# Optimization experiments

Measured on AMD Instinct MI355X. Metric: run time of the kernel, lower is better.

The kernel has to match this reference:

```python
import jax, jax.numpy as jnp
import numpy as np

B, N, C = 2, 9216, 512
HEAD, SR = 8, 4
R = 32  # lora rank
SCALING = 4.0 / 32.0  # alpha / r


def setup_inputs() -> dict:
    key = jax.random.key(0)
    ks = jax.random.split(key, 16)
    s = 0.02
    inp = {
        "x": jax.random.normal(ks[0], (B, N, C), jnp.float32),
        "w_q": jax.random.normal(ks[1], (C, C), jnp.float32) * s,
        "b_q": jnp.zeros((C,), jnp.float32),
        "w_kv": jax.random.normal(ks[2], (2 * C, C), jnp.float32) * s,
        "b_kv": jnp.zeros((2 * C,), jnp.float32),
        "w_proj": jax.random.normal(ks[3], (C, C), jnp.float32) * s,
        "b_proj": jnp.zeros((C,), jnp.float32),
        "w_sr": jax.random.normal(ks[4], (C, C, SR, SR), jnp.float32) * s,
        "b_sr": jnp.zeros((C,), jnp.float32),
        "ln_g": jnp.ones((C,), jnp.float32),
        "ln_b": jnp.zeros((C,), jnp.float32),
        "lora_A_q": jax.random.normal(ks[5], (R, C), jnp.float32) * s,
        "lora_B_q": jax.random.normal(ks[6], (C, R), jnp.float32) * s,
        "lora_A_v": jax.random.normal(ks[7], (R, C), jnp.float32) * s,
        "lora_B_v": jax.random.normal(ks[8], (C, R), jnp.float32) * s,
        "H": 96,
        "W": 96,
    }
    return inp


def reference(x, w_q, b_q, w_kv, b_kv, w_proj, b_proj, w_sr, b_sr,
              ln_g, ln_b, lora_A_q, lora_B_q, lora_A_v, lora_B_v, H, W):
    b, n, c = x.shape
    d = c // HEAD
    # q = Linear(x) + LoRA(x) * scaling
    q = x @ w_q.T + b_q + ((x @ lora_A_q.T) @ lora_B_q.T) * SCALING
    q = q.reshape(b, n, HEAD, d).transpose(0, 2, 1, 3)  # (B, h, N, d)
    # spatial reduction: Conv2d(dim, dim, sr, sr) then LayerNorm
    xi = x.transpose(0, 2, 1).reshape(b, c, H, W)
    xs = jax.lax.conv_general_dilated(
        xi, w_sr, window_strides=(SR, SR), padding='VALID',
        dimension_numbers=('NCHW', 'OIHW', 'NCHW'))
    xs = xs + b_sr[None, :, None, None]
    xs = xs.reshape(b, c, -1).transpose(0, 2, 1)  # (B, Nkv, C)
    mu = jnp.mean(xs, axis=-1, keepdims=True)
    var = jnp.var(xs, axis=-1, keepdims=True)
    xs = (xs - mu) * jax.lax.rsqrt(var + 1e-5) * ln_g + ln_b
    # k, v
    kv = (xs @ w_kv.T + b_kv).reshape(b, -1, 2, HEAD, d).transpose(2, 0, 3, 1, 4)
    k, v = kv[0], kv[1]  # (B, h, Nkv, d)
    lv = ((xs @ lora_A_v.T) @ lora_B_v.T) * SCALING  # (B, Nkv, C)
    # faithful to torch: raw memory reshape, NOT a head-transpose
    v = v + lv.reshape(b, HEAD, -1, d)
    # attention
    attn = jax.nn.softmax(jnp.einsum('bhnd,bhmd->bhnm', q, k) * (d ** -0.5), axis=-1)
    out = jnp.einsum('bhnm,bhmd->bhnd', attn, v).transpose(0, 2, 1, 3).reshape(b, n, c)
    return out @ w_proj.T + b_proj
```

## Files before the change

kernel.cpp:

```cpp
#include <hip/hip_runtime.h>

typedef __attribute__((ext_vector_type(8))) __bf16 bf16x8;
typedef __attribute__((ext_vector_type(4))) float f32x4;
typedef __attribute__((ext_vector_type(4))) unsigned int u32x4;
typedef __attribute__((ext_vector_type(2))) unsigned int u32x2;

#define MFMA16(a, b, c) __builtin_amdgcn_mfma_f32_16x16x32_bf16((a), (b), (c), 0, 0, 0)
#define QSCALE 0.18033688011112042f

__device__ __forceinline__ bool input_is_f32(const void* ln_g) {
    return ((const unsigned*)ln_g)[0] == 0x3F800000u;
}

__device__ __forceinline__ float rdf(const void* p, long i, bool f32) {
    return f32 ? ((const float*)p)[i] : (float)((const __bf16*)p)[i];
}

__device__ __forceinline__ void conv_big(const void* s, __bf16* d, long base, bool f) {
    long i = base + (long)threadIdx.x * 8;
    if (f) {
        f32x4 a = ((const f32x4*)s)[i / 4];
        f32x4 b = ((const f32x4*)s)[i / 4 + 1];
        bf16x8 o;
        #pragma unroll
        for (int j = 0; j < 4; ++j) { o[j] = (__bf16)a[j]; o[4 + j] = (__bf16)b[j]; }
        *(bf16x8*)(d + i) = o;
    } else {
        *(u32x4*)(d + i) = ((const u32x4*)s)[i / 8];
    }
}

__device__ __forceinline__ void conv_small(const void* s, __bf16* d, int n, bool f) {
    int i = threadIdx.x * 4;
    if (i < n) {
        #pragma unroll
        for (int j = 0; j < 4; ++j)
            d[i + j] = f ? (__bf16)((const float*)s)[i + j] : ((const __bf16*)s)[i + j];
    }
}

__global__ void convert_prep_kernel(const void* x, const void* w_kv, const void* w_proj,
                                    const void* b_q, const void* b_kv, const void* b_proj,
                                    const void* b_sr, const void* ln_g, const void* ln_b,
                                    const void* __restrict__ w_q,
                                    const void* __restrict__ Aq, const void* __restrict__ Bq,
                                    const void* __restrict__ Av, const void* __restrict__ Bv,
                                    const void* __restrict__ w_sr,
                                    __bf16* x_b, __bf16* w_kv_b, __bf16* w_proj_b,
                                    __bf16* b_q_b, __bf16* b_kv_b, __bf16* b_proj_b,
                                    __bf16* b_sr_b, __bf16* ln_g_b, __bf16* ln_b_b,
                                    __bf16* __restrict__ w_q_eff, __bf16* __restrict__ w_lv,
                                    __bf16* __restrict__ w_sr_t) {
    const bool f = input_is_f32(ln_g);
    int blk = blockIdx.x;
    if (blk < 4608)      conv_big(x, x_b, (long)blk * 2048, f);
    else if (blk < 4864) conv_big(w_kv, w_kv_b, (long)(blk - 4608) * 2048, f);
    else if (blk < 4992) conv_big(w_proj, w_proj_b, (long)(blk - 4864) * 2048, f);
    else if (blk == 4992) conv_small(b_q, b_q_b, 512, f);
    else if (blk == 4993) conv_small(b_kv, b_kv_b, 1024, f);
    else if (blk == 4994) conv_small(b_proj, b_proj_b, 512, f);
    else if (blk == 4995) conv_small(b_sr, b_sr_b, 512, f);
    else if (blk == 4996) conv_small(ln_g, ln_g_b, 512, f);
    else if (blk == 4997) conv_small(ln_b, ln_b_b, 512, f);
    else {
        int tid = (blk - 4998) * 256 + threadIdx.x;
        if (tid < 262144) {
            int o = tid >> 9, c = tid & 511;
            float acc = 0.f;
            #pragma unroll 8
            for (int r = 0; r < 32; ++r)
                acc += rdf(Bq, o * 32 + r, f) * rdf(Aq, r * 512 + c, f);
            w_q_eff[tid] = (__bf16)(rdf(w_q, tid, f) + 0.125f * acc);
        } else if (tid < 524288) {
            int t = tid - 262144;
            int o = t >> 9, c = t & 511;
            float acc = 0.f;
            #pragma unroll 8
            for (int r = 0; r < 32; ++r)
                acc += rdf(Bv, o * 32 + r, f) * rdf(Av, r * 512 + c, f);
            w_lv[t] = (__bf16)(0.125f * acc);
        } else if (tid < 786432) {
            int t = tid - 524288;
            int o = t >> 9, i = t & 511;
            #pragma unroll
            for (int p = 0; p < 16; ++p)
                w_sr_t[(size_t)o * 8192 + p * 512 + i] = (__bf16)rdf(w_sr, (long)t * 16 + p, f);
        }
    }
}

__global__ __launch_bounds__(256, 4) void qconv_gemm(const __bf16* __restrict__ x,
                                                     const __bf16* __restrict__ Wt,
                                                     const __bf16* __restrict__ Wq,
                                                     const __bf16* __restrict__ bq,
                                                     float* __restrict__ part,
                                                     __bf16* __restrict__ q_t) {
    __shared__ __attribute__((aligned(16))) char lds[36864];
    char* As = lds;
    char* Bs = lds + 18432;
    const int tid = threadIdx.x;
    const int swz = (blockIdx.x & 7) * 144 + (blockIdx.x >> 3);
    const bool isconv = (swz & 1) == 0;
    const int hid = swz >> 1;
    const int w = tid >> 6, lane = tid & 63;
    const int wm = (w >> 1) << 6, wn = (w & 1) << 6;
    const int lr = lane & 15, lg = lane >> 4;
    const int srow = tid >> 1, half = tid & 1;

    int m0, n0, kzv = 0;
    const __bf16 *Arow, *Brow;
    if (isconv) {
        kzv = hid / 36;
        int r = hid % 36;
        int nb = r / 9, mb = r % 9;
        m0 = mb << 7; n0 = nb << 7;
        int m = m0 + srow;
        int bb = m >= 576 ? 1 : 0;
        int rem = m - bb * 576;
        int oy = rem / 24;
        int ox = rem - oy * 24;
        int ky = kzv >> 2, kx = kzv & 3;
        Arow = x + ((size_t)bb * 9216 + (size_t)(oy * 384 + ky * 96 + ox * 4 + kx)) * 512
               + half * 32;
        Brow = Wt + (size_t)(n0 + srow) * 8192 + kzv * 512 + half * 32;
    } else {
        int mb = hid >> 2, nb = hid & 3;
        m0 = mb << 7; n0 = nb << 7;
        Arow = x + (size_t)(m0 + srow) * 512 + half * 32;
        Brow = Wq + (size_t)(n0 + srow) * 512 + half * 32;
    }
    char* Asw = As + srow * 144 + half * 64;
    char* Bsw = Bs + srow * 144 + half * 64;

    f32x4 acc[4][4] = {};

    u32x4 a0 = *(const u32x4*)(Arow);
    u32x4 a1 = *(const u32x4*)(Arow + 8);
    u32x4 a2 = *(const u32x4*)(Arow + 16);
    u32x4 a3 = *(const u32x4*)(Arow + 24);
    u32x4 b0 = *(const u32x4*)(Brow);
    u32x4 b1 = *(const u32x4*)(Brow + 8);
    u32x4 b2 = *(const u32x4*)(Brow + 16);
    u32x4 b3 = *(const u32x4*)(Brow + 24);

    for (int k0 = 0; k0 < 512; k0 += 64) {
        __syncthreads();
        *(u32x4*)(Asw) = a0;
        *(u32x4*)(Asw + 16) = a1;
        *(u32x4*)(Asw + 32) = a2;
        *(u32x4*)(Asw + 48) = a3;
        *(u32x4*)(Bsw) = b0;
        *(u32x4*)(Bsw + 16) = b1;
        *(u32x4*)(Bsw + 32) = b2;
        *(u32x4*)(Bsw + 48) = b3;
        __syncthreads();
        int kn = k0 + 64;
        if (kn < 512) {
            a0 = *(const u32x4*)(Arow + kn);
            a1 = *(const u32x4*)(Arow + kn + 8);
            a2 = *(const u32x4*)(Arow + kn + 16);
            a3 = *(const u32x4*)(Arow + kn + 24);
            b0 = *(const u32x4*)(Brow + kn);
            b1 = *(const u32x4*)(Brow + kn + 8);
            b2 = *(const u32x4*)(Brow + kn + 16);
            b3 = *(const u32x4*)(Brow + kn + 24);
        }
        bf16x8 a[4][2], b[4][2];
        #pragma unroll
        for (int i = 0; i < 4; ++i)
            #pragma unroll
            for (int ks = 0; ks < 2; ++ks)
                a[i][ks] = *(const bf16x8*)(As + (wm + i * 16 + lr) * 144 + ks * 64 + lg * 16);
        #pragma unroll
        for (int j = 0; j < 4; ++j)
            #pragma unroll
            for (int ks = 0; ks < 2; ++ks)
                b[j][ks] = *(const bf16x8*)(Bs + (wn + j * 16 + lr) * 144 + ks * 64 + lg * 16);
        #pragma unroll
        for (int i = 0; i < 4; ++i)
            #pragma unroll
            for (int j = 0; j < 4; ++j)
                #pragma unroll
                for (int ks = 0; ks < 2; ++ks)
                    acc[i][j] = MFMA16(a[i][ks], b[j][ks], acc[i][j]);
    }

    if (isconv) {
        float* pout = part + (size_t)kzv * 589824;
        #pragma unroll
        for (int j = 0; j < 4; ++j) {
            int col = n0 + wn + j * 16 + lr;
            #pragma unroll
            for (int i = 0; i < 4; ++i) {
                int rb = m0 + wm + i * 16 + lg * 4;
                #pragma unroll
                for (int r = 0; r < 4; ++r)
                    pout[(size_t)(rb + r) * 512 + col] = acc[i][j][r];
            }
        }
    } else {
        #pragma unroll
        for (int j = 0; j < 4; ++j) {
            int col = n0 + wn + j * 16 + lr;
            float bv = (float)bq[col];
            #pragma unroll
            for (int i = 0; i < 4; ++i) {
                int rb = m0 + wm + i * 16 + lg * 4;
                #pragma unroll
                for (int r = 0; r < 4; ++r) {
                    int grow = rb + r;
                    int b_ = grow >= 9216 ? 1 : 0;
                    int nn = grow - b_ * 9216;
                    q_t[(((size_t)(b_ * 8 + (col >> 6))) * 9216 + nn) * 64 + (col & 63)] =
                        (__bf16)((acc[i][j][r] + bv) * QSCALE);
                }
            }
        }
    }
}

__global__ __launch_bounds__(256, 4) void proj_gemm(const __bf16* __restrict__ A,
                                                    const __bf16* __restrict__ Bt,
                                                    const __bf16* __restrict__ bias,
                                                    float* __restrict__ out) {
    __shared__ __attribute__((aligned(16))) char lds[27648];
    char* As = lds;
    char* Bs = lds + 9216;
    const int tid = threadIdx.x;
    const int swz = (blockIdx.x & 7) * 144 + (blockIdx.x >> 3);
    const int m0 = (swz >> 2) << 6, n0 = (swz & 3) << 7;
    const int w = tid >> 6, lane = tid & 63;
    const int wm = (w >> 1) << 5, wn = (w & 1) << 6;
    const int lr = lane & 15, lg = lane >> 4;

    f32x4 acc[2][4] = {};

    const int srow = tid >> 1, half = tid & 1;
    const bool doA = tid < 128;
    const __bf16* Arow = A + (size_t)(m0 + (srow & 63)) * 512 + half * 32;
    const __bf16* Brow = Bt + (size_t)(n0 + srow) * 512 + half * 32;
    char* Asw = As + (srow & 63) * 144 + half * 64;
    char* Bsw = Bs + srow * 144 + half * 64;

    u32x4 a0{}, a1{}, a2{}, a3{};
    if (doA) {
        a0 = *(const u32x4*)(Arow);
        a1 = *(const u32x4*)(Arow + 8);
        a2 = *(const u32x4*)(Arow + 16);
        a3 = *(const u32x4*)(Arow + 24);
    }
    u32x4 b0 = *(const u32x4*)(Brow);
    u32x4 b1 = *(const u32x4*)(Brow + 8);
    u32x4 b2 = *(const u32x4*)(Brow + 16);
    u32x4 b3 = *(const u32x4*)(Brow + 24);

    for (int k0 = 0; k0 < 512; k0 += 64) {
        __syncthreads();
        if (doA) {
            *(u32x4*)(Asw) = a0;
            *(u32x4*)(Asw + 16) = a1;
            *(u32x4*)(Asw + 32) = a2;
            *(u32x4*)(Asw + 48) = a3;
        }
        *(u32x4*)(Bsw) = b0;
        *(u32x4*)(Bsw + 16) = b1;
        *(u32x4*)(Bsw + 32) = b2;
        *(u32x4*)(Bsw + 48) = b3;
        __syncthreads();
        int kn = k0 + 64;
        if (kn < 512) {
            if (doA) {
                a0 = *(const u32x4*)(Arow + kn);
                a1 = *(const u32x4*)(Arow + kn + 8);
                a2 = *(const u32x4*)(Arow + kn + 16);
                a3 = *(const u32x4*)(Arow + kn + 24);
            }
            b0 = *(const u32x4*)(Brow + kn);
            b1 = *(const u32x4*)(Brow + kn + 8);
            b2 = *(const u32x4*)(Brow + kn + 16);
            b3 = *(const u32x4*)(Brow + kn + 24);
        }
        bf16x8 a[2][2], b[4][2];
        #pragma unroll
        for (int i = 0; i < 2; ++i)
            #pragma unroll
            for (int ks = 0; ks < 2; ++ks)
                a[i][ks] = *(const bf16x8*)(As + (wm + i * 16 + lr) * 144 + ks * 64 + lg * 16);
        #pragma unroll
        for (int j = 0; j < 4; ++j)
            #pragma unroll
            for (int ks = 0; ks < 2; ++ks)
                b[j][ks] = *(const bf16x8*)(Bs + (wn + j * 16 + lr) * 144 + ks * 64 + lg * 16);
        #pragma unroll
        for (int i = 0; i < 2; ++i)
            #pragma unroll
            for (int j = 0; j < 4; ++j)
                #pragma unroll
                for (int ks = 0; ks < 2; ++ks)
                    acc[i][j] = MFMA16(a[i][ks], b[j][ks], acc[i][j]);
    }

    #pragma unroll
    for (int j = 0; j < 4; ++j) {
        int col = n0 + wn + j * 16 + lr;
        float bv = (float)bias[col];
        #pragma unroll
        for (int i = 0; i < 2; ++i) {
            int rb = m0 + wm + i * 16 + lg * 4;
            #pragma unroll
            for (int r = 0; r < 4; ++r)
                out[(size_t)(rb + r) * 512 + col] = acc[i][j][r] + bv;
        }
    }
}

__global__ __launch_bounds__(64) void lnorm(const float* __restrict__ parts,
                                            const __bf16* __restrict__ b_sr,
                                            const __bf16* __restrict__ g,
                                            const __bf16* __restrict__ be,
                                            __bf16* __restrict__ out) {
    int row = blockIdx.x;
    int lane = threadIdx.x;
    const float* xr = parts + (size_t)row * 512;
    float v[8], s = 0.f, sq = 0.f;
    #pragma unroll
    for (int i = 0; i < 8; ++i) {
        int c = lane + i * 64;
        float t = (float)b_sr[c];
        #pragma unroll
        for (int sp = 0; sp < 16; ++sp)
            t += xr[(size_t)sp * 589824 + c];
        v[i] = t;
        s += t;
        sq += t * t;
    }
    #pragma unroll
    for (int d = 1; d < 64; d <<= 1) {
        s += __shfl_xor(s, d);
        sq += __shfl_xor(sq, d);
    }
    float mean = s * (1.0f / 512.0f);
    float var = sq * (1.0f / 512.0f) - mean * mean;
    float rstd = rsqrtf(var + 1e-5f);
    __bf16* orow = out + (size_t)row * 512;
    #pragma unroll
    for (int i = 0; i < 8; ++i) {
        int c = lane + i * 64;
        orow[c] = (__bf16)((v[i] - mean) * rstd * (float)g[c] + (float)be[c]);
    }
}

__global__ __launch_bounds__(256) void kv_gemm(const __bf16* __restrict__ xs,
                                               const __bf16* __restrict__ w_kv,
                                               const __bf16* __restrict__ w_lv,
                                               const __bf16* __restrict__ b_kv,
                                               __bf16* __restrict__ k_t,
                                               float* __restrict__ v_raw,
                                               __bf16* __restrict__ lv) {
    __shared__ __attribute__((aligned(16))) char lds[18432];
    char* As = lds;
    char* Bs = lds + 9216;
    const int tid = threadIdx.x;
    const int m0 = blockIdx.x << 6, n0 = blockIdx.y << 6;
    const int w = tid >> 6, lane = tid & 63;
    const int wm = (w >> 1) << 5, wn = (w & 1) << 5;
    const int lr = lane & 15, lg = lane >> 4;

    const int srow = tid >> 2, sc = tid & 3;
    const __bf16* arow = xs + (size_t)(m0 + srow) * 512;
    const __bf16* brow = (n0 < 1024) ? (w_kv + (size_t)(n0 + srow) * 512)
                                     : (w_lv + (size_t)(n0 - 1024 + srow) * 512);

    u32x4 pav[2], pbv[2];
    #pragma unroll
    for (int j = 0; j < 2; ++j) {
        int c = sc + j * 4;
        pav[j] = *(const u32x4*)(arow + c * 8);
        pbv[j] = *(const u32x4*)(brow + c * 8);
    }

    f32x4 acc[2][2] = {};
    for (int k0 = 0; k0 < 512; k0 += 64) {
        __syncthreads();
        #pragma unroll
        for (int j = 0; j < 2; ++j) {
            int c = sc + j * 4;
            *(u32x4*)(As + srow * 144 + c * 16) = pav[j];
            *(u32x4*)(Bs + srow * 144 + c * 16) = pbv[j];
        }
        __syncthreads();
        int kn = k0 + 64;
        if (kn < 512) {
            #pragma unroll
            for (int j = 0; j < 2; ++j) {
                int c = sc + j * 4;
                pav[j] = *(const u32x4*)(arow + kn + c * 8);
                pbv[j] = *(const u32x4*)(brow + kn + c * 8);
            }
        }
        bf16x8 a[2][2], b[2][2];
        #pragma unroll
        for (int i = 0; i < 2; ++i)
            #pragma unroll
            for (int ks = 0; ks < 2; ++ks) {
                a[i][ks] = *(const bf16x8*)(As + (wm + i * 16 + lr) * 144 + ks * 64 + lg * 16);
                b[i][ks] = *(const bf16x8*)(Bs + (wn + i * 16 + lr) * 144 + ks * 64 + lg * 16);
            }
        #pragma unroll
        for (int i = 0; i < 2; ++i)
            #pragma unroll
            for (int j = 0; j < 2; ++j)
                #pragma unroll
                for (int ks = 0; ks < 2; ++ks)
                    acc[i][j] = MFMA16(a[i][ks], b[j][ks], acc[i][j]);
    }
    #pragma unroll
    for (int j = 0; j < 2; ++j) {
        int col = n0 + wn + j * 16 + lr;
        float bv = (col < 1024) ? (float)b_kv[col] : 0.0f;
        #pragma unroll
        for (int i = 0; i < 2; ++i) {
            int rb = m0 + wm + i * 16 + lg * 4;
            #pragma unroll
            for (int r = 0; r < 4; ++r) {
                int grow = rb + r;
                float val = acc[i][j][r] + bv;
                int b_ = grow >= 576 ? 1 : 0;
                int mm = grow - b_ * 576;
                if (col < 512) {
                    int h = col >> 6, dd = col & 63;
                    k_t[(((size_t)(b_ * 8 + h)) * 576 + mm) * 64 + dd] = (__bf16)val;
                } else if (col < 1024) {
                    v_raw[((size_t)b_ * 576 + mm) * 512 + (col - 512)] = val;
                } else {
                    lv[((size_t)b_ * 576 + mm) * 512 + (col - 1024)] = (__bf16)val;
                }
            }
        }
    }
}

__global__ void v_fixup(const float* __restrict__ v_raw, const __bf16* __restrict__ lv,
                        __bf16* __restrict__ vT) {
    int tid = blockIdx.x * 256 + threadIdx.x;
    if (tid >= 589824) return;
    int mm = tid % 576;
    int rest = tid / 576;
    int dd = rest & 63;
    int bh = rest >> 6;
    int b_ = bh >> 3, h = bh & 7;
    int flat = h * 36864 + mm * 64 + dd;
    int n2 = flat >> 9, c2 = flat & 511;
    float val = v_raw[((size_t)b_ * 576 + mm) * 512 + h * 64 + dd] +
                (float)lv[((size_t)b_ * 576 + n2) * 512 + c2];
    vT[tid] = (__bf16)val;
}

__global__ __launch_bounds__(256, 4) void attn_kernel(const __bf16* __restrict__ q_t,
                                                      const __bf16* __restrict__ k_t,
                                                      const __bf16* __restrict__ vT,
                                                      __bf16* __restrict__ attnv) {
    __shared__ __attribute__((aligned(16))) char lds[18432];
    char* Ks = lds;
    char* Vs = lds + 9216;
    const int tid = threadIdx.x;
    const int w = tid >> 6, lane = tid & 63;
    const int lr = lane & 15, lg = lane >> 4;
    const int bh = blockIdx.y;
    const int qrow0 = (blockIdx.x << 7) + (w << 5);

    bf16x8 qf[2][2];
    #pragma unroll
    for (int qb = 0; qb < 2; ++qb)
        #pragma unroll
        for (int ks = 0; ks < 2; ++ks)
            qf[qb][ks] = *(const bf16x8*)(q_t + ((size_t)bh * 9216 + qrow0 + qb * 16 + lr) * 64 +
                                          ks * 32 + lg * 8);

    bf16x8 ones;
    #pragma unroll
    for (int j = 0; j < 8; ++j) ones[j] = (__bf16)1.0f;

    f32x4 oacc[2][4] = {};
    f32x4 lacc[2] = {};

    const int rr = tid >> 2, q4 = tid & 3;
    const __bf16* kg = k_t + ((size_t)bh * 576 + rr) * 64 + q4 * 16;
    char* ksw = Ks + rr * 144 + q4 * 32;
    const __bf16* vg = vT + ((size_t)bh * 64 + rr) * 576 + q4 * 16;
    char* vsw = Vs + rr * 144;
    const int offA = ((q4 & 1) << 3) | ((q4 >> 1) << 6);

    u32x4 k0v = *(const u32x4*)(kg);
    u32x4 k1v = *(const u32x4*)(kg + 8);
    u32x4 v0v = *(const u32x4*)(vg);
    u32x4 v1v = *(const u32x4*)(vg + 8);

    for (int kv0 = 0; kv0 < 576; kv0 += 64) {
        __syncthreads();
        *(u32x4*)(ksw) = k0v;
        *(u32x4*)(ksw + 16) = k1v;
        {
            u32x2 t0, t1, t2, t3;
            t0[0] = v0v[0]; t0[1] = v0v[1];
            t1[0] = v0v[2]; t1[1] = v0v[3];
            t2[0] = v1v[0]; t2[1] = v1v[1];
            t3[0] = v1v[2]; t3[1] = v1v[3];
            *(u32x2*)(vsw + offA) = t0;
            *(u32x2*)(vsw + offA + 16) = t1;
            *(u32x2*)(vsw + offA + 32) = t2;
            *(u32x2*)(vsw + offA + 48) = t3;
        }
        __syncthreads();
        int kvn = kv0 + 64;
        if (kvn < 576) {
            k0v = *(const u32x4*)(kg + (size_t)kvn * 64);
            k1v = *(const u32x4*)(kg + (size_t)kvn * 64 + 8);
            v0v = *(const u32x4*)(vg + kvn);
            v1v = *(const u32x4*)(vg + kvn + 8);
        }

        #pragma unroll
        for (int ch = 0; ch < 2; ++ch) {
            bf16x8 kf[2][2];
            #pragma unroll
            for (int kb = 0; kb < 2; ++kb)
                #pragma unroll
                for (int ks = 0; ks < 2; ++ks)
                    kf[kb][ks] = *(const bf16x8*)(Ks + ((ch * 2 + kb) * 16 + lr) * 144 +
                                                  ks * 64 + lg * 16);
            f32x4 st[2][2] = {};
            #pragma unroll
            for (int kb = 0; kb < 2; ++kb)
                #pragma unroll
                for (int qb = 0; qb < 2; ++qb)
                    #pragma unroll
                    for (int ks = 0; ks < 2; ++ks)
                        st[kb][qb] = MFMA16(kf[kb][ks], qf[qb][ks], st[kb][qb]);
            bf16x8 vf[4];
            #pragma unroll
            for (int nd = 0; nd < 4; ++nd)
                vf[nd] = *(const bf16x8*)(Vs + (nd * 16 + lr) * 144 + ch * 64 + lg * 16);
            #pragma unroll
            for (int qb = 0; qb < 2; ++qb) {
                bf16x8 pa;
                #pragma unroll
                for (int kb = 0; kb < 2; ++kb)
                    #pragma unroll
                    for (int r = 0; r < 4; ++r)
                        pa[kb * 4 + r] = (__bf16)__builtin_amdgcn_exp2f(st[kb][qb][r]);
                #pragma unroll
                for (int nd = 0; nd < 4; ++nd)
                    oacc[qb][nd] = MFMA16(pa, vf[nd], oacc[qb][nd]);
                lacc[qb] = MFMA16(pa, ones, lacc[qb]);
            }
        }
    }

    const int b_ = bh >> 3, h = bh & 7;
    #pragma unroll
    for (int qb = 0; qb < 2; ++qb) {
        f32x4 linv;
        #pragma unroll
        for (int r = 0; r < 4; ++r) linv[r] = 1.0f / lacc[qb][r];
        #pragma unroll
        for (int nd = 0; nd < 4; ++nd)
            #pragma unroll
            for (int r = 0; r < 4; ++r) {
                int row = qrow0 + qb * 16 + lg * 4 + r;
                int col = h * 64 + nd * 16 + lr;
                attnv[((size_t)b_ * 9216 + row) * 512 + col] =
                    (__bf16)(oacc[qb][nd][r] * linv[r]);
            }
    }
}

extern "C" void kernel_launch(void* const* d_in, const int* in_sizes, int n_in,
                              void* d_out, int out_size, void* d_ws, size_t ws_size,
                              hipStream_t stream) {
    const void* x      = d_in[0];
    const void* w_q    = d_in[1];
    const void* b_q    = d_in[2];
    const void* w_kv   = d_in[3];
    const void* b_kv   = d_in[4];
    const void* w_proj = d_in[5];
    const void* b_proj = d_in[6];
    const void* w_sr   = d_in[7];
    const void* b_sr   = d_in[8];
    const void* ln_g   = d_in[9];
    const void* ln_b   = d_in[10];
    const void* A_q    = d_in[11];
    const void* B_q    = d_in[12];
    const void* A_v    = d_in[13];
    const void* B_v    = d_in[14];

    char* ws = (char*)d_ws;
    __bf16* x_b      = (__bf16*)(ws);
    __bf16* attnv    = (__bf16*)(ws);
    __bf16* q_t      = (__bf16*)(ws + 18874368);
    __bf16* k_t      = (__bf16*)(ws + 37748736);
    __bf16* vT       = (__bf16*)(ws + 38928384);
    __bf16* w_q_eff  = (__bf16*)(ws + 40108032);
    __bf16* w_lv     = (__bf16*)(ws + 40632320);
    __bf16* w_sr_t   = (__bf16*)(ws + 41156608);
    __bf16* w_kv_b   = (__bf16*)(ws + 49545216);
    __bf16* w_proj_b = (__bf16*)(ws + 50593792);
    __bf16* xs_ln    = (__bf16*)(ws + 53477376);
    float*  v_raw    = (float*)(ws + 54657024);
    __bf16* lv       = (__bf16*)(ws + 57016320);
    __bf16* b_q_b    = (__bf16*)(ws + 58195968);
    __bf16* b_kv_b   = (__bf16*)(ws + 58196992);
    __bf16* b_proj_b = (__bf16*)(ws + 58199040);
    __bf16* b_sr_b   = (__bf16*)(ws + 58200064);
    __bf16* ln_g_b   = (__bf16*)(ws + 58201088);
    __bf16* ln_b_b   = (__bf16*)(ws + 58202112);
    float*  parts    = (float*)(ws + 58204160);

    convert_prep_kernel<<<8070, 256, 0, stream>>>(
        x, w_kv, w_proj, b_q, b_kv, b_proj, b_sr, ln_g, ln_b,
        w_q, A_q, B_q, A_v, B_v, w_sr,
        x_b, w_kv_b, w_proj_b, b_q_b, b_kv_b, b_proj_b, b_sr_b, ln_g_b, ln_b_b,
        w_q_eff, w_lv, w_sr_t);
    qconv_gemm<<<1152, 256, 0, stream>>>(x_b, w_sr_t, w_q_eff, b_q_b, parts, q_t);
    lnorm<<<1152, 64, 0, stream>>>(parts, b_sr_b, ln_g_b, ln_b_b, xs_ln);
    kv_gemm<<<dim3(18, 24), 256, 0, stream>>>(xs_ln, w_kv_b, w_lv, b_kv_b, k_t, v_raw, lv);
    v_fixup<<<2304, 256, 0, stream>>>(v_raw, lv, vT);
    attn_kernel<<<dim3(72, 16), 256, 0, stream>>>(q_t, k_t, vT, attnv);
    proj_gemm<<<1152, 256, 0, stream>>>(attnv, w_proj_b, b_proj_b, (float*)d_out);
}
```

Before: 247.7 us.

## Restructure conv split-K to 4 partitions with 64-row tiles and XCD-aware block mapping

The spatial-reduction conv GEMM drops from 16 split-K partitions of K=512 to 4 partitions of K=2048, each covering one kernel row with a 64x128 tile. The q GEMM and conv blocks are interleaved 1:2 and mapped by XCD, so each XCD works on a contiguous range of q rows and a fixed conv kz slice, which should improve L2 locality. With fewer partials, lnorm sums 4 slices instead of 16, cutting partial-buffer traffic. The launch shrinks to 864 blocks and kv_gemm gets an occupancy hint. The trade-offs are longer serial K loops per conv block and half of the threads idling during A tile loads.

```diff
diff --git a/kernel.cpp b/kernel.cpp
--- a/kernel.cpp
+++ b/kernel.cpp
@@ -99,99 +99,99 @@
     char* As = lds;
     char* Bs = lds + 18432;
     const int tid = threadIdx.x;
-    const int swz = (blockIdx.x & 7) * 144 + (blockIdx.x >> 3);
-    const bool isconv = (swz & 1) == 0;
-    const int hid = swz >> 1;
+    const int xcd = blockIdx.x & 7;
+    const int p = blockIdx.x >> 3;
+    const bool isconv = (p % 3) == 0;
     const int w = tid >> 6, lane = tid & 63;
-    const int wm = (w >> 1) << 6, wn = (w & 1) << 6;
     const int lr = lane & 15, lg = lane >> 4;
     const int srow = tid >> 1, half = tid & 1;
 
-    int m0, n0, kzv = 0;
-    const __bf16 *Arow, *Brow;
     if (isconv) {
-        kzv = hid / 36;
-        int r = hid % 36;
-        int nb = r / 9, mb = r % 9;
-        m0 = mb << 7; n0 = nb << 7;
-        int m = m0 + srow;
+        const int c = p / 3;
+        const int kz = xcd >> 1;
+        const int mb = c >> 1;
+        const int nb = ((xcd & 1) << 1) | (c & 1);
+        const int m0 = mb << 6, n0 = nb << 7;
+        const int wm = (w >> 1) << 5, wn = (w & 1) << 6;
+
+        const bool doA = tid < 128;
+        int m = m0 + (srow & 63);
         int bb = m >= 576 ? 1 : 0;
         int rem = m - bb * 576;
         int oy = rem / 24;
         int ox = rem - oy * 24;
-        int ky = kzv >> 2, kx = kzv & 3;
-        Arow = x + ((size_t)bb * 9216 + (size_t)(oy * 384 + ky * 96 + ox * 4 + kx)) * 512
-               + half * 32;
-        Brow = Wt + (size_t)(n0 + srow) * 8192 + kzv * 512 + half * 32;
-    } else {
-        int mb = hid >> 2, nb = hid & 3;
-        m0 = mb << 7; n0 = nb << 7;
-        Arow = x + (size_t)(m0 + srow) * 512 + half * 32;
-        Brow = Wq + (size_t)(n0 + srow) * 512 + half * 32;
-    }
-    char* Asw = As + srow * 144 + half * 64;
-    char* Bsw = Bs + srow * 144 + half * 64;
-
-    f32x4 acc[4][4] = {};
-
-    u32x4 a0 = *(const u32x4*)(Arow);
-    u32x4 a1 = *(const u32x4*)(Arow + 8);
-    u32x4 a2 = *(const u32x4*)(Arow + 16);
-    u32x4 a3 = *(const u32x4*)(Arow + 24);
-    u32x4 b0 = *(const u32x4*)(Brow);
-    u32x4 b1 = *(const u32x4*)(Brow + 8);
-    u32x4 b2 = *(const u32x4*)(Brow + 16);
-    u32x4 b3 = *(const u32x4*)(Brow + 24);
-
-    for (int k0 = 0; k0 < 512; k0 += 64) {
-        __syncthreads();
-        *(u32x4*)(Asw) = a0;
-        *(u32x4*)(Asw + 16) = a1;
-        *(u32x4*)(Asw + 32) = a2;
-        *(u32x4*)(Asw + 48) = a3;
-        *(u32x4*)(Bsw) = b0;
-        *(u32x4*)(Bsw + 16) = b1;
-        *(u32x4*)(Bsw + 32) = b2;
-        *(u32x4*)(Bsw + 48) = b3;
-        __syncthreads();
-        int kn = k0 + 64;
-        if (kn < 512) {
-            a0 = *(const u32x4*)(Arow + kn);
-            a1 = *(const u32x4*)(Arow + kn + 8);
-            a2 = *(const u32x4*)(Arow + kn + 16);
-            a3 = *(const u32x4*)(Arow + kn + 24);
-            b0 = *(const u32x4*)(Brow + kn);
-            b1 = *(const u32x4*)(Brow + kn + 8);
-            b2 = *(const u32x4*)(Brow + kn + 16);
-            b3 = *(const u32x4*)(Brow + kn + 24);
-        }
-        bf16x8 a[4][2], b[4][2];
-        #pragma unroll
-        for (int i = 0; i < 4; ++i)
-            #pragma unroll
-            for (int ks = 0; ks < 2; ++ks)
-                a[i][ks] = *(const bf16x8*)(As + (wm + i * 16 + lr) * 144 + ks * 64 + lg * 16);
-        #pragma unroll
-        for (int j = 0; j < 4; ++j)
-            #pragma unroll
-            for (int ks = 0; ks < 2; ++ks)
-                b[j][ks] = *(const bf16x8*)(Bs + (wn + j * 16 + lr) * 144 + ks * 64 + lg * 16);
-        #pragma unroll
-        for (int i = 0; i < 4; ++i)
+        const __bf16* Arow = x + ((size_t)bb * 9216 + (size_t)(oy * 384 + kz * 96 + ox * 4)) * 512
+                             + half * 32;
+        const __bf16* Brow = Wt + (size_t)(n0 + srow) * 8192 + kz * 2048 + half * 32;
+        char* Asw = As + (srow & 63) * 144 + half * 64;
+        char* Bsw = Bs + srow * 144 + half * 64;
+
+        f32x4 acc[2][4] = {};
+
+        u32x4 a0{}, a1{}, a2{}, a3{};
+        if (doA) {
+            a0 = *(const u32x4*)(Arow);
+            a1 = *(const u32x4*)(Arow + 8);
+            a2 = *(const u32x4*)(Arow + 16);
+            a3 = *(const u32x4*)(Arow + 24);
+        }
+        u32x4 b0 = *(const u32x4*)(Brow);
+        u32x4 b1 = *(const u32x4*)(Brow + 8);
+        u32x4 b2 = *(const u32x4*)(Brow + 16);
+        u32x4 b3 = *(const u32x4*)(Brow + 24);
+
+        for (int k0 = 0; k0 < 2048; k0 += 64) {
+            __syncthreads();
+            if (doA) {
+                *(u32x4*)(Asw) = a0;
+                *(u32x4*)(Asw + 16) = a1;
+                *(u32x4*)(Asw + 32) = a2;
+                *(u32x4*)(Asw + 48) = a3;
+            }
+            *(u32x4*)(Bsw) = b0;
+            *(u32x4*)(Bsw + 16) = b1;
+            *(u32x4*)(Bsw + 32) = b2;
+            *(u32x4*)(Bsw + 48) = b3;
+            __syncthreads();
+            int kn = k0 + 64;
+            if (kn < 2048) {
+                if (doA) {
+                    a0 = *(const u32x4*)(Arow + kn);
+                    a1 = *(const u32x4*)(Arow + kn + 8);
+                    a2 = *(const u32x4*)(Arow + kn + 16);
+                    a3 = *(const u32x4*)(Arow + kn + 24);
+                }
+                b0 = *(const u32x4*)(Brow + kn);
+                b1 = *(const u32x4*)(Brow + kn + 8);
+                b2 = *(const u32x4*)(Brow + kn + 16);
+                b3 = *(const u32x4*)(Brow + kn + 24);
+            }
+            bf16x8 a[2][2], b[4][2];
+            #pragma unroll
+            for (int i = 0; i < 2; ++i)
+                #pragma unroll
+                for (int ks = 0; ks < 2; ++ks)
+                    a[i][ks] = *(const bf16x8*)(As + (wm + i * 16 + lr) * 144 + ks * 64 + lg * 16);
             #pragma unroll
             for (int j = 0; j < 4; ++j)
                 #pragma unroll
                 for (int ks = 0; ks < 2; ++ks)
-                    acc[i][j] = MFMA16(a[i][ks], b[j][ks], acc[i][j]);
-    }
-
-    if (isconv) {
-        float* pout = part + (size_t)kzv * 589824;
+                    b[j][ks] = *(const bf16x8*)(Bs + (wn + j * 16 + lr) * 144 + ks * 64 + lg * 16);
+            #pragma unroll
+            for (int i = 0; i < 2; ++i)
+                #pragma unroll
+                for (int j = 0; j < 4; ++j)
+                    #pragma unroll
+                    for (int ks = 0; ks < 2; ++ks)
+                        acc[i][j] = MFMA16(a[i][ks], b[j][ks], acc[i][j]);
+        }
+
+        float* pout = part + (size_t)kz * 589824;
         #pragma unroll
         for (int j = 0; j < 4; ++j) {
             int col = n0 + wn + j * 16 + lr;
             #pragma unroll
-            for (int i = 0; i < 4; ++i) {
+            for (int i = 0; i < 2; ++i) {
                 int rb = m0 + wm + i * 16 + lg * 4;
                 #pragma unroll
                 for (int r = 0; r < 4; ++r)
@@ -199,6 +199,70 @@
             }
         }
     } else {
+        const int qi = (p / 3) * 2 + (p % 3 - 1);
+        const int mb = xcd * 18 + (qi >> 2);
+        const int nb = qi & 3;
+        const int m0 = mb << 7, n0 = nb << 7;
+        const int wm = (w >> 1) << 6, wn = (w & 1) << 6;
+
+        const __bf16* Arow = x + (size_t)(m0 + srow) * 512 + half * 32;
+        const __bf16* Brow = Wq + (size_t)(n0 + srow) * 512 + half * 32;
+        char* Asw = As + srow * 144 + half * 64;
+        char* Bsw = Bs + srow * 144 + half * 64;
+
+        f32x4 acc[4][4] = {};
+
+        u32x4 a0 = *(const u32x4*)(Arow);
+        u32x4 a1 = *(const u32x4*)(Arow + 8);
+        u32x4 a2 = *(const u32x4*)(Arow + 16);
+        u32x4 a3 = *(const u32x4*)(Arow + 24);
+        u32x4 b0 = *(const u32x4*)(Brow);
+        u32x4 b1 = *(const u32x4*)(Brow + 8);
+        u32x4 b2 = *(const u32x4*)(Brow + 16);
+        u32x4 b3 = *(const u32x4*)(Brow + 24);
+
+        for (int k0 = 0; k0 < 512; k0 += 64) {
+            __syncthreads();
+            *(u32x4*)(Asw) = a0;
+            *(u32x4*)(Asw + 16) = a1;
+            *(u32x4*)(Asw + 32) = a2;
+            *(u32x4*)(Asw + 48) = a3;
+            *(u32x4*)(Bsw) = b0;
+            *(u32x4*)(Bsw + 16) = b1;
+            *(u32x4*)(Bsw + 32) = b2;
+            *(u32x4*)(Bsw + 48) = b3;
+            __syncthreads();
+            int kn = k0 + 64;
+            if (kn < 512) {
+                a0 = *(const u32x4*)(Arow + kn);
+                a1 = *(const u32x4*)(Arow + kn + 8);
+                a2 = *(const u32x4*)(Arow + kn + 16);
+                a3 = *(const u32x4*)(Arow + kn + 24);
+                b0 = *(const u32x4*)(Brow + kn);
+                b1 = *(const u32x4*)(Brow + kn + 8);
+                b2 = *(const u32x4*)(Brow + kn + 16);
+                b3 = *(const u32x4*)(Brow + kn + 24);
+            }
+            bf16x8 a[4][2], b[4][2];
+            #pragma unroll
+            for (int i = 0; i < 4; ++i)
+                #pragma unroll
+                for (int ks = 0; ks < 2; ++ks)
+                    a[i][ks] = *(const bf16x8*)(As + (wm + i * 16 + lr) * 144 + ks * 64 + lg * 16);
+            #pragma unroll
+            for (int j = 0; j < 4; ++j)
+                #pragma unroll
+                for (int ks = 0; ks < 2; ++ks)
+                    b[j][ks] = *(const bf16x8*)(Bs + (wn + j * 16 + lr) * 144 + ks * 64 + lg * 16);
+            #pragma unroll
+            for (int i = 0; i < 4; ++i)
+                #pragma unroll
+                for (int j = 0; j < 4; ++j)
+                    #pragma unroll
+                    for (int ks = 0; ks < 2; ++ks)
+                        acc[i][j] = MFMA16(a[i][ks], b[j][ks], acc[i][j]);
+        }
+
         #pragma unroll
         for (int j = 0; j < 4; ++j) {
             int col = n0 + wn + j * 16 + lr;
@@ -328,7 +392,7 @@
         int c = lane + i * 64;
         float t = (float)b_sr[c];
         #pragma unroll
-        for (int sp = 0; sp < 16; ++sp)
+        for (int sp = 0; sp < 4; ++sp)
             t += xr[(size_t)sp * 589824 + c];
         v[i] = t;
         s += t;
@@ -350,13 +414,13 @@
     }
 }
 
-__global__ __launch_bounds__(256) void kv_gemm(const __bf16* __restrict__ xs,
-                                               const __bf16* __restrict__ w_kv,
-                                               const __bf16* __restrict__ w_lv,
-                                               const __bf16* __restrict__ b_kv,
-                                               __bf16* __restrict__ k_t,
-                                               float* __restrict__ v_raw,
-                                               __bf16* __restrict__ lv) {
+__global__ __launch_bounds__(256, 4) void kv_gemm(const __bf16* __restrict__ xs,
+                                                  const __bf16* __restrict__ w_kv,
+                                                  const __bf16* __restrict__ w_lv,
+                                                  const __bf16* __restrict__ b_kv,
+                                                  __bf16* __restrict__ k_t,
+                                                  float* __restrict__ v_raw,
+                                                  __bf16* __restrict__ lv) {
     __shared__ __attribute__((aligned(16))) char lds[18432];
     char* As = lds;
     char* Bs = lds + 9216;
@@ -621,7 +685,7 @@
         w_q, A_q, B_q, A_v, B_v, w_sr,
         x_b, w_kv_b, w_proj_b, b_q_b, b_kv_b, b_proj_b, b_sr_b, ln_g_b, ln_b_b,
         w_q_eff, w_lv, w_sr_t);
-    qconv_gemm<<<1152, 256, 0, stream>>>(x_b, w_sr_t, w_q_eff, b_q_b, parts, q_t);
+    qconv_gemm<<<864, 256, 0, stream>>>(x_b, w_sr_t, w_q_eff, b_q_b, parts, q_t);
     lnorm<<<1152, 64, 0, stream>>>(parts, b_sr_b, ln_g_b, ln_b_b, xs_ln);
     kv_gemm<<<dim3(18, 24), 256, 0, stream>>>(xs_ln, w_kv_b, w_lv, b_kv_b, k_t, v_raw, lv);
     v_fixup<<<2304, 256, 0, stream>>>(v_raw, lv, vT);
```

After: 282.2 us. +13.9%, slower.

## Fuse x fp32-to-bf16 conversion into qconv GEMM loads and vectorize layernorm

Applied to the files above, without the earlier changes.

The separate pass that converts x into a bf16 workspace copy is removed. The q/conv GEMM now reads the original fp32 x directly and converts to bf16 in registers while loading tiles. This avoids writing and rereading a 19MB intermediate, at the cost of doubling the A-operand global read bytes per tile and adding conversion instructions. The layernorm kernel is also rewritten to use 8-wide vector loads and stores per lane, and kv_gemm gets an occupancy hint in its launch bounds.

```diff
diff --git a/kernel.cpp b/kernel.cpp
--- a/kernel.cpp
+++ b/kernel.cpp
@@ -14,6 +14,27 @@
 
 __device__ __forceinline__ float rdf(const void* p, long i, bool f32) {
     return f32 ? ((const float*)p)[i] : (float)((const __bf16*)p)[i];
+}
+
+__device__ __forceinline__ void ld32(const void* x, size_t eoff, bool f,
+                                     u32x4& r0, u32x4& r1, u32x4& r2, u32x4& r3) {
+    if (f) {
+        const f32x4* p = (const f32x4*)((const float*)x + eoff);
+        f32x4 v0 = p[0], v1 = p[1], v2 = p[2], v3 = p[3];
+        f32x4 v4 = p[4], v5 = p[5], v6 = p[6], v7 = p[7];
+        bf16x8 o0, o1, o2, o3;
+        #pragma unroll
+        for (int j = 0; j < 4; ++j) {
+            o0[j] = (__bf16)v0[j]; o0[4 + j] = (__bf16)v1[j];
+            o1[j] = (__bf16)v2[j]; o1[4 + j] = (__bf16)v3[j];
+            o2[j] = (__bf16)v4[j]; o2[4 + j] = (__bf16)v5[j];
+            o3[j] = (__bf16)v6[j]; o3[4 + j] = (__bf16)v7[j];
+        }
+        r0 = *(u32x4*)&o0; r1 = *(u32x4*)&o1; r2 = *(u32x4*)&o2; r3 = *(u32x4*)&o3;
+    } else {
+        const u32x4* p = (const u32x4*)((const __bf16*)x + eoff);
+        r0 = p[0]; r1 = p[1]; r2 = p[2]; r3 = p[3];
+    }
 }
 
 __device__ __forceinline__ void conv_big(const void* s, __bf16* d, long base, bool f) {
@@ -39,31 +60,30 @@
     }
 }
 
-__global__ void convert_prep_kernel(const void* x, const void* w_kv, const void* w_proj,
+__global__ void convert_prep_kernel(const void* w_kv, const void* w_proj,
                                     const void* b_q, const void* b_kv, const void* b_proj,
                                     const void* b_sr, const void* ln_g, const void* ln_b,
                                     const void* __restrict__ w_q,
                                     const void* __restrict__ Aq, const void* __restrict__ Bq,
                                     const void* __restrict__ Av, const void* __restrict__ Bv,
                                     const void* __restrict__ w_sr,
-                                    __bf16* x_b, __bf16* w_kv_b, __bf16* w_proj_b,
+                                    __bf16* w_kv_b, __bf16* w_proj_b,
                                     __bf16* b_q_b, __bf16* b_kv_b, __bf16* b_proj_b,
                                     __bf16* b_sr_b, __bf16* ln_g_b, __bf16* ln_b_b,
                                     __bf16* __restrict__ w_q_eff, __bf16* __restrict__ w_lv,
                                     __bf16* __restrict__ w_sr_t) {
     const bool f = input_is_f32(ln_g);
     int blk = blockIdx.x;
-    if (blk < 4608)      conv_big(x, x_b, (long)blk * 2048, f);
-    else if (blk < 4864) conv_big(w_kv, w_kv_b, (long)(blk - 4608) * 2048, f);
-    else if (blk < 4992) conv_big(w_proj, w_proj_b, (long)(blk - 4864) * 2048, f);
-    else if (blk == 4992) conv_small(b_q, b_q_b, 512, f);
-    else if (blk == 4993) conv_small(b_kv, b_kv_b, 1024, f);
-    else if (blk == 4994) conv_small(b_proj, b_proj_b, 512, f);
-    else if (blk == 4995) conv_small(b_sr, b_sr_b, 512, f);
-    else if (blk == 4996) conv_small(ln_g, ln_g_b, 512, f);
-    else if (blk == 4997) conv_small(ln_b, ln_b_b, 512, f);
+    if (blk < 256)       conv_big(w_kv, w_kv_b, (long)blk * 2048, f);
+    else if (blk < 384)  conv_big(w_proj, w_proj_b, (long)(blk - 256) * 2048, f);
+    else if (blk == 384) conv_small(b_q, b_q_b, 512, f);
+    else if (blk == 385) conv_small(b_kv, b_kv_b, 1024, f);
+    else if (blk == 386) conv_small(b_proj, b_proj_b, 512, f);
+    else if (blk == 387) conv_small(b_sr, b_sr_b, 512, f);
+    else if (blk == 388) conv_small(ln_g, ln_g_b, 512, f);
+    else if (blk == 389) conv_small(ln_b, ln_b_b, 512, f);
     else {
-        int tid = (blk - 4998) * 256 + threadIdx.x;
+        int tid = (blk - 390) * 256 + threadIdx.x;
         if (tid < 262144) {
             int o = tid >> 9, c = tid & 511;
             float acc = 0.f;
@@ -89,7 +109,8 @@
     }
 }
 
-__global__ __launch_bounds__(256, 4) void qconv_gemm(const __bf16* __restrict__ x,
+__global__ __launch_bounds__(256, 4) void qconv_gemm(const void* __restrict__ x,
+                                                     const void* __restrict__ lng,
                                                      const __bf16* __restrict__ Wt,
                                                      const __bf16* __restrict__ Wq,
                                                      const __bf16* __restrict__ bq,
@@ -98,6 +119,7 @@
     __shared__ __attribute__((aligned(16))) char lds[36864];
     char* As = lds;
     char* Bs = lds + 18432;
+    const bool f = input_is_f32(lng);
     const int tid = threadIdx.x;
     const int swz = (blockIdx.x & 7) * 144 + (blockIdx.x >> 3);
     const bool isconv = (swz & 1) == 0;
@@ -108,7 +130,8 @@
     const int srow = tid >> 1, half = tid & 1;
 
     int m0, n0, kzv = 0;
-    const __bf16 *Arow, *Brow;
+    size_t aoff;
+    const __bf16* Brow;
     if (isconv) {
         kzv = hid / 36;
         int r = hid % 36;
@@ -120,13 +143,13 @@
         int oy = rem / 24;
         int ox = rem - oy * 24;
         int ky = kzv >> 2, kx = kzv & 3;
-        Arow = x + ((size_t)bb * 9216 + (size_t)(oy * 384 + ky * 96 + ox * 4 + kx)) * 512
+        aoff = ((size_t)bb * 9216 + (size_t)(oy * 384 + ky * 96 + ox * 4 + kx)) * 512
                + half * 32;
         Brow = Wt + (size_t)(n0 + srow) * 8192 + kzv * 512 + half * 32;
     } else {
         int mb = hid >> 2, nb = hid & 3;
         m0 = mb << 7; n0 = nb << 7;
-        Arow = x + (size_t)(m0 + srow) * 512 + half * 32;
+        aoff = (size_t)(m0 + srow) * 512 + half * 32;
         Brow = Wq + (size_t)(n0 + srow) * 512 + half * 32;
     }
     char* Asw = As + srow * 144 + half * 64;
@@ -134,10 +157,8 @@
 
     f32x4 acc[4][4] = {};
 
-    u32x4 a0 = *(const u32x4*)(Arow);
-    u32x4 a1 = *(const u32x4*)(Arow + 8);
-    u32x4 a2 = *(const u32x4*)(Arow + 16);
-    u32x4 a3 = *(const u32x4*)(Arow + 24);
+    u32x4 a0, a1, a2, a3;
+    ld32(x, aoff, f, a0, a1, a2, a3);
     u32x4 b0 = *(const u32x4*)(Brow);
     u32x4 b1 = *(const u32x4*)(Brow + 8);
     u32x4 b2 = *(const u32x4*)(Brow + 16);
@@ -156,10 +177,7 @@
         __syncthreads();
         int kn = k0 + 64;
         if (kn < 512) {
-            a0 = *(const u32x4*)(Arow + kn);
-            a1 = *(const u32x4*)(Arow + kn + 8);
-            a2 = *(const u32x4*)(Arow + kn + 16);
-            a3 = *(const u32x4*)(Arow + kn + 24);
+            ld32(x, aoff + kn, f, a0, a1, a2, a3);
             b0 = *(const u32x4*)(Brow + kn);
             b1 = *(const u32x4*)(Brow + kn + 8);
             b2 = *(const u32x4*)(Brow + kn + 16);
@@ -321,19 +339,21 @@
                                             __bf16* __restrict__ out) {
     int row = blockIdx.x;
     int lane = threadIdx.x;
-    const float* xr = parts + (size_t)row * 512;
-    float v[8], s = 0.f, sq = 0.f;
-    #pragma unroll
-    for (int i = 0; i < 8; ++i) {
-        int c = lane + i * 64;
-        float t = (float)b_sr[c];
-        #pragma unroll
-        for (int sp = 0; sp < 16; ++sp)
-            t += xr[(size_t)sp * 589824 + c];
-        v[i] = t;
-        s += t;
-        sq += t * t;
-    }
+    const float* xr = parts + (size_t)row * 512 + lane * 8;
+    float v[8];
+    bf16x8 bs = *(const bf16x8*)(b_sr + lane * 8);
+    #pragma unroll
+    for (int j = 0; j < 8; ++j) v[j] = (float)bs[j];
+    #pragma unroll
+    for (int sp = 0; sp < 16; ++sp) {
+        f32x4 p0 = *(const f32x4*)(xr + (size_t)sp * 589824);
+        f32x4 p1 = *(const f32x4*)(xr + (size_t)sp * 589824 + 4);
+        #pragma unroll
+        for (int j = 0; j < 4; ++j) { v[j] += p0[j]; v[4 + j] += p1[j]; }
+    }
+    float s = 0.f, sq = 0.f;
+    #pragma unroll
+    for (int j = 0; j < 8; ++j) { s += v[j]; sq += v[j] * v[j]; }
     #pragma unroll
     for (int d = 1; d < 64; d <<= 1) {
         s += __shfl_xor(s, d);
@@ -342,21 +362,22 @@
     float mean = s * (1.0f / 512.0f);
     float var = sq * (1.0f / 512.0f) - mean * mean;
     float rstd = rsqrtf(var + 1e-5f);
-    __bf16* orow = out + (size_t)row * 512;
-    #pragma unroll
-    for (int i = 0; i < 8; ++i) {
-        int c = lane + i * 64;
-        orow[c] = (__bf16)((v[i] - mean) * rstd * (float)g[c] + (float)be[c]);
-    }
-}
-
-__global__ __launch_bounds__(256) void kv_gemm(const __bf16* __restrict__ xs,
-                                               const __bf16* __restrict__ w_kv,
-                                               const __bf16* __restrict__ w_lv,
-                                               const __bf16* __restrict__ b_kv,
-                                               __bf16* __restrict__ k_t,
-                                               float* __restrict__ v_raw,
-                                               __bf16* __restrict__ lv) {
+    bf16x8 gg = *(const bf16x8*)(g + lane * 8);
+    bf16x8 bb = *(const bf16x8*)(be + lane * 8);
+    bf16x8 o;
+    #pragma unroll
+    for (int j = 0; j < 8; ++j)
+        o[j] = (__bf16)((v[j] - mean) * rstd * (float)gg[j] + (float)bb[j]);
+    *(bf16x8*)(out + (size_t)row * 512 + lane * 8) = o;
+}
+
+__global__ __launch_bounds__(256, 4) void kv_gemm(const __bf16* __restrict__ xs,
+                                                  const __bf16* __restrict__ w_kv,
+                                                  const __bf16* __restrict__ w_lv,
+                                                  const __bf16* __restrict__ b_kv,
+                                                  __bf16* __restrict__ k_t,
+                                                  float* __restrict__ v_raw,
+                                                  __bf16* __restrict__ lv) {
     __shared__ __attribute__((aligned(16))) char lds[18432];
     char* As = lds;
     char* Bs = lds + 9216;
@@ -595,7 +616,6 @@
     const void* B_v    = d_in[14];
 
     char* ws = (char*)d_ws;
-    __bf16* x_b      = (__bf16*)(ws);
     __bf16* attnv    = (__bf16*)(ws);
     __bf16* q_t      = (__bf16*)(ws + 18874368);
     __bf16* k_t      = (__bf16*)(ws + 37748736);
@@ -616,12 +636,12 @@
     __bf16* ln_b_b   = (__bf16*)(ws + 58202112);
     float*  parts    = (float*)(ws + 58204160);
 
-    convert_prep_kernel<<<8070, 256, 0, stream>>>(
-        x, w_kv, w_proj, b_q, b_kv, b_proj, b_sr, ln_g, ln_b,
+    convert_prep_kernel<<<3462, 256, 0, stream>>>(
+        w_kv, w_proj, b_q, b_kv, b_proj, b_sr, ln_g, ln_b,
         w_q, A_q, B_q, A_v, B_v, w_sr,
-        x_b, w_kv_b, w_proj_b, b_q_b, b_kv_b, b_proj_b, b_sr_b, ln_g_b, ln_b_b,
+        w_kv_b, w_proj_b, b_q_b, b_kv_b, b_proj_b, b_sr_b, ln_g_b, ln_b_b,
         w_q_eff, w_lv, w_sr_t);
-    qconv_gemm<<<1152, 256, 0, stream>>>(x_b, w_sr_t, w_q_eff, b_q_b, parts, q_t);
+    qconv_gemm<<<1152, 256, 0, stream>>>(x, ln_g, w_sr_t, w_q_eff, b_q_b, parts, q_t);
     lnorm<<<1152, 64, 0, stream>>>(parts, b_sr_b, ln_g_b, ln_b_b, xs_ln);
     kv_gemm<<<dim3(18, 24), 256, 0, stream>>>(xs_ln, w_kv_b, w_lv, b_kv_b, k_t, v_raw, lv);
     v_fixup<<<2304, 256, 0, stream>>>(v_raw, lv, vT);
```

Result: slower. 305.1 us (+23.2%).
